# Performance work log

Measured on AMD Instinct MI355X. Metric: run time of the kernel, lower is better.

The kernel has to match this reference:

```python
import jax, jax.numpy as jnp
import numpy as np
from jax import lax

MODES = 16
DEPTH = 8
NPH = 8  # photons = sum(init_state); init_state = [1]*8 + [0]*8
IDX = np.arange(NPH)  # output_indices derived from init_state
PI = np.pi
CHUNK = 4096  # pairs per permanent chunk (memory control, mirrors chunk_subsets idea)


def setup_inputs() -> dict:
    key = jax.random.key(0)
    k1, k2, k3 = jax.random.split(key, 3)
    x = jax.random.normal(k1, (256, 64), dtype=jnp.float32)
    W = jax.random.normal(k2, (120, 64), dtype=jnp.float32) / np.sqrt(64.0)
    b = jax.random.normal(k3, (120,), dtype=jnp.float32) * 0.01
    return {"x": x, "W": W, "b": b}


def _forward(x, W, b):
    N = x.shape[0]
    # fc1 + sigmoid embedding -> angle pairs
    x_emb = jax.nn.sigmoid(x @ W.T + b)              # (N, 120)
    tbu = x_emb.reshape(N, -1, 2)                    # (N, T, 2)
    theta = tbu[:, :, 0] * (PI / 2)
    phi = tbu[:, :, 1] * (2 * PI)
    ct = jnp.cos(theta).astype(jnp.complex64)
    st = jnp.sin(theta).astype(jnp.complex64)
    ep = jnp.exp(1j * phi.astype(jnp.complex64))
    # 2x2 tunable beam-splitter unitaries: [[e^{i phi} c, -s], [e^{i phi} s, c]]
    row0 = jnp.stack([ep * ct, -st], axis=-1)
    row1 = jnp.stack([ep * st, ct], axis=-1)
    blocks = jnp.stack([row0, row1], axis=-2)        # (N, T, 2, 2)

    # Apply block-diagonal layers. Block-diag matmul only mixes row pairs,
    # so update row segments directly instead of building (modes,modes) UBS.
    U = jnp.broadcast_to(jnp.eye(MODES, dtype=jnp.complex64), (N, MODES, MODES))
    nb_even, nb_odd = MODES // 2, (MODES - 2) // 2
    n_before = 0
    for d in range(DEPTH):
        if d % 2 == 0:
            nb, off = nb_even, 0
        else:
            nb, off = nb_odd, 1
        blk = blocks[:, n_before:n_before + nb]                      # (N, nb, 2, 2)
        seg = U[:, off:off + 2 * nb, :].reshape(N, nb, 2, MODES)     # row pairs
        new = jnp.einsum('nkab,nkbm->nkam', blk, seg).reshape(N, 2 * nb, MODES)
        U = U.at[:, off:off + 2 * nb, :].set(new)
        n_before += nb

    # Photonic Gram: K[a,b] = |perm( (U_a^dag U_b)[idx, idx] )|^2.
    # Only the idx-columns of U enter: V = U[:, :, idx], submatrix = V_a^dag V_b.
    V = U[:, :, IDX]                                  # (N, MODES, n)
    G = jnp.einsum('ami,bmj->abij', V.conj(), V)      # (N, N, n, n)

    n = NPH
    subsets = jnp.arange(1, 1 << n)                   # (S,), S = 2^n - 1
    masks = (subsets[:, None] >> jnp.arange(n)[None, :]) & 1   # (S, n)
    signs = (1 - 2 * ((n - masks.sum(axis=1)) & 1)).astype(jnp.complex64)
    maskc = masks.astype(jnp.complex64)

    A = G.reshape(N * N, n, n)
    nc = (N * N) // CHUNK

    def perm_chunk(Ac):  # Ryser: sum_S (-1)^{n-|S|} prod_i sum_{j in S} A_ij
        ss = jnp.einsum('cij,sj->csi', Ac, maskc)     # (c, S, n) subset row-sums
        pr = jnp.prod(ss, axis=2)                     # (c, S)
        return jnp.sum(pr * signs, axis=1)            # (c,)

    perms = lax.map(perm_chunk, A.reshape(nc, CHUNK, n, n)).reshape(N * N)
    K = (jnp.abs(perms) ** 2).astype(jnp.float32).reshape(N, N)
    di = jnp.arange(N)
    K = K.at[di, di].set(1.0)
    return x_emb, K


def reference(x, W, b):
    return _forward(x, W, b)
```

## Files before the change

kernel.cpp:

```cpp
#include <hip/hip_runtime.h>
#include <math.h>

#define NS 256
#define EMB 120
#define NBLK 60
#define MODES 16
#define NPH 8

__device__ __forceinline__ float2 cmul(float2 a, float2 b) {
    float2 r;
    r.x = fmaf(a.x, b.x, -(a.y * b.y));
    r.y = fmaf(a.x, b.y,   a.y * b.x);
    return r;
}

__global__ __launch_bounds__(128) void emb_v_kernel(
    const float* __restrict__ x, const float* __restrict__ W,
    const float* __restrict__ bias, float* __restrict__ out_emb,
    float2* __restrict__ Vws)
{
    const int s = blockIdx.x;
    const int t = threadIdx.x;
    __shared__ float emb[EMB];
    __shared__ float ctA[NBLK], stA[NBLK], exA[NBLK], eyA[NBLK];

    if (t < EMB) {
        const float* xr = x + s * 64;
        const float* wr = W + t * 64;
        float acc = bias[t];
        #pragma unroll
        for (int k = 0; k < 64; ++k) acc = fmaf(xr[k], wr[k], acc);
        float e = 1.0f / (1.0f + expf(-acc));
        emb[t] = e;
        out_emb[s * EMB + t] = e;
    }
    __syncthreads();

    if (t < NBLK) {
        float th = emb[2 * t]     * 1.57079632679489662f;
        float ph = emb[2 * t + 1] * 6.28318530717958648f;
        float st, ct, sp, cp;
        sincosf(th, &st, &ct);
        sincosf(ph, &sp, &cp);
        ctA[t] = ct; stA[t] = st; exA[t] = cp; eyA[t] = sp;
    }
    __syncthreads();

    if (t < NPH) {
        const int c = t;
        float2 u[MODES];
        #pragma unroll
        for (int m = 0; m < MODES; ++m) {
            u[m].x = (m == c) ? 1.0f : 0.0f;
            u[m].y = 0.0f;
        }
        int bi = 0;
        #pragma unroll
        for (int d = 0; d < 8; ++d) {
            const int off = d & 1;
            const int nb = 8 - off;
            #pragma unroll
            for (int k = 0; k < nb; ++k) {
                float ct = ctA[bi], st = stA[bi], ex = exA[bi], ey = eyA[bi];
                ++bi;
                const int r0 = off + 2 * k;
                float2 u0 = u[r0], u1 = u[r0 + 1];
                float2 n0, n1;
                n0.x = ex * ct * u0.x - ey * ct * u0.y - st * u1.x;
                n0.y = ex * ct * u0.y + ey * ct * u0.x - st * u1.y;
                n1.x = ex * st * u0.x - ey * st * u0.y + ct * u1.x;
                n1.y = ex * st * u0.y + ey * st * u0.x + ct * u1.y;
                u[r0] = n0; u[r0 + 1] = n1;
            }
        }
        #pragma unroll
        for (int m = 0; m < MODES; ++m)
            Vws[(s * MODES + m) * NPH + c] = u[m];
    }
}

__global__ __launch_bounds__(256, 1) void perm_kernel(
    const float2* __restrict__ Vws, float* __restrict__ outK)
{
    __shared__ float2 sva[8][132];
    __shared__ float2 svb[8][132];
    __shared__ float2 sG[64][66];

    const int tid = threadIdx.x;
    const int ta = blockIdx.x >> 5;
    const int tb = blockIdx.x & 31;

    const float4* srcA = (const float4*)(Vws + (size_t)ta * 8 * 128);
    const float4* srcB = (const float4*)(Vws + (size_t)tb * 8 * 128);
    #pragma unroll
    for (int r = 0; r < 2; ++r) {
        int idx = r * 256 + tid;
        int row = idx >> 6;
        int c4  = idx & 63;
        *(float4*)&sva[row][c4 * 2] = srcA[idx];
        *(float4*)&svb[row][c4 * 2] = srcB[idx];
    }
    __syncthreads();

    const int p  = tid >> 2;
    const int q  = tid & 3;
    const int pa = p >> 3;
    const int pb = p & 7;

    float2 Ga[2][8];
    #pragma unroll
    for (int i = 0; i < 2; ++i)
        #pragma unroll
        for (int j = 0; j < 8; ++j) { Ga[i][j].x = 0.f; Ga[i][j].y = 0.f; }

    #pragma unroll 1
    for (int m = 0; m < 16; ++m) {
        float4 va4 = *(const float4*)&sva[pa][m * 8 + 2 * q];
        float2 a0; a0.x = va4.x; a0.y = va4.y;
        float2 a1; a1.x = va4.z; a1.y = va4.w;
        float2 vb[8];
        #pragma unroll
        for (int jj = 0; jj < 4; ++jj) {
            float4 b4 = *(const float4*)&svb[pb][m * 8 + 2 * jj];
            vb[2 * jj].x     = b4.x; vb[2 * jj].y     = b4.y;
            vb[2 * jj + 1].x = b4.z; vb[2 * jj + 1].y = b4.w;
        }
        #pragma unroll
        for (int j = 0; j < 8; ++j) {
            Ga[0][j].x = fmaf(a0.x, vb[j].x, fmaf(a0.y, vb[j].y, Ga[0][j].x));
            Ga[0][j].y = fmaf(a0.x, vb[j].y, fmaf(-a0.y, vb[j].x, Ga[0][j].y));
            Ga[1][j].x = fmaf(a1.x, vb[j].x, fmaf(a1.y, vb[j].y, Ga[1][j].x));
            Ga[1][j].y = fmaf(a1.x, vb[j].y, fmaf(-a1.y, vb[j].x, Ga[1][j].y));
        }
    }
    #pragma unroll
    for (int i = 0; i < 2; ++i)
        #pragma unroll
        for (int jj = 0; jj < 4; ++jj) {
            float4 w;
            w.x = Ga[i][2 * jj].x;     w.y = Ga[i][2 * jj].y;
            w.z = Ga[i][2 * jj + 1].x; w.w = Ga[i][2 * jj + 1].y;
            *(float4*)&sG[p][(2 * q + i) * 8 + 2 * jj] = w;
        }
    __syncthreads();

    float2 G[8][8];
    #pragma unroll
    for (int i = 0; i < 8; ++i)
        #pragma unroll
        for (int jj = 0; jj < 4; ++jj) {
            float4 g4 = *(const float4*)&sG[p][i * 8 + 2 * jj];
            G[i][2 * jj].x     = g4.x; G[i][2 * jj].y     = g4.y;
            G[i][2 * jj + 1].x = g4.z; G[i][2 * jj + 1].y = g4.w;
        }

    const float d6 = (q & 1) ? -1.f : 1.f;
    const float d7 = (q & 2) ? -1.f : 1.f;

    float2 rs[8];
    #pragma unroll
    for (int i = 0; i < 8; ++i) {
        float sx = G[i][0].x + G[i][1].x + G[i][2].x + G[i][3].x + G[i][4].x + G[i][5].x;
        float sy = G[i][0].y + G[i][1].y + G[i][2].y + G[i][3].y + G[i][4].y + G[i][5].y;
        sx = fmaf(d6, G[i][6].x, sx); sx = fmaf(d7, G[i][7].x, sx);
        sy = fmaf(d6, G[i][6].y, sy); sy = fmaf(d7, G[i][7].y, sy);
        rs[i].x = sx; rs[i].y = sy;
    }

    float2 acc;

#define PRODTREE(OUT) do {                                            \
        float2 p01 = cmul(rs[0], rs[1]);                              \
        float2 p23 = cmul(rs[2], rs[3]);                              \
        float2 p45 = cmul(rs[4], rs[5]);                              \
        float2 p67 = cmul(rs[6], rs[7]);                              \
        float2 q0  = cmul(p01, p23);                                  \
        float2 q1  = cmul(p45, p67);                                  \
        OUT = cmul(q0, q1);                                           \
    } while (0)

#define UPD(J, S) do {                                                \
        _Pragma("unroll")                                             \
        for (int i = 0; i < 8; ++i) {                                 \
            rs[i].x = fmaf((S), G[i][J].x, rs[i].x);                  \
            rs[i].y = fmaf((S), G[i][J].y, rs[i].y);                  \
        }                                                             \
    } while (0)

#define TERM(TS) do {                                                 \
        float2 pr; PRODTREE(pr);                                      \
        acc.x = fmaf((TS), pr.x, acc.x);                              \
        acc.y = fmaf((TS), pr.y, acc.y);                              \
    } while (0)

    PRODTREE(acc);
    UPD(1, -2.f); TERM(-1.f);
    UPD(2, -2.f); TERM( 1.f);
    UPD(1,  2.f); TERM(-1.f);
    UPD(3, -2.f); TERM( 1.f);
    UPD(1, -2.f); TERM(-1.f);
    UPD(2,  2.f); TERM( 1.f);
    UPD(1,  2.f); TERM(-1.f);
    UPD(4, -2.f); TERM( 1.f);
    UPD(1, -2.f); TERM(-1.f);
    UPD(2, -2.f); TERM( 1.f);
    UPD(1,  2.f); TERM(-1.f);
    UPD(3,  2.f); TERM( 1.f);
    UPD(1, -2.f); TERM(-1.f);
    UPD(2,  2.f); TERM( 1.f);
    UPD(1,  2.f); TERM(-1.f);
    UPD(5, -2.f); TERM( 1.f);
    UPD(1, -2.f); TERM(-1.f);
    UPD(2, -2.f); TERM( 1.f);
    UPD(1,  2.f); TERM(-1.f);
    UPD(3, -2.f); TERM( 1.f);
    UPD(1, -2.f); TERM(-1.f);
    UPD(2,  2.f); TERM( 1.f);
    UPD(1,  2.f); TERM(-1.f);
    UPD(4,  2.f); TERM( 1.f);
    UPD(1, -2.f); TERM(-1.f);
    UPD(2, -2.f); TERM( 1.f);
    UPD(1,  2.f); TERM(-1.f);
    UPD(3,  2.f); TERM( 1.f);
    UPD(1, -2.f); TERM(-1.f);
    UPD(2,  2.f); TERM( 1.f);
    UPD(1,  2.f); TERM(-1.f);
#undef UPD
#undef TERM
#undef PRODTREE

    const float sq = d6 * d7;
    float ax = acc.x * sq, ay = acc.y * sq;
    ax += __shfl_xor(ax, 1); ay += __shfl_xor(ay, 1);
    ax += __shfl_xor(ax, 2); ay += __shfl_xor(ay, 2);

    if (q == 0) {
        const int a = ta * 8 + pa;
        const int b = tb * 8 + pb;
        float K = fmaf(ax, ax, ay * ay) * (1.0f / 16384.0f);
        if (a == b) K = 1.0f;
        outK[a * 256 + b] = K;
    }
}

extern "C" void kernel_launch(void* const* d_in, const int* in_sizes, int n_in,
                              void* d_out, int out_size, void* d_ws, size_t ws_size,
                              hipStream_t stream) {
    const float* x    = (const float*)d_in[0];
    const float* W    = (const float*)d_in[1];
    const float* bias = (const float*)d_in[2];
    float* out     = (float*)d_out;
    float* out_emb = out;
    float* outK    = out + NS * EMB;
    float2* Vws    = (float2*)d_ws;

    emb_v_kernel<<<NS, 128, 0, stream>>>(x, W, bias, out_emb, Vws);
    perm_kernel<<<1024, 256, 0, stream>>>(Vws, outK);
}
```

Measured before the change: 82.34 us.

## Exploit Gram symmetry with triangular tiles and split permanent rows across lanes

Launches only upper-triangular tile pairs (528 blocks) and writes each K value to both (a,b) and (b,a), relying on |perm(G^H)| = |perm(G)| to roughly halve the work. Each pair now uses 8 lanes instead of 4, each holding 4 rows; the 8-row product is completed with a DPP xor-1 exchange, and the final reduction uses DPP plus a shuffle. Shared memory for the V tiles is aliased onto the G buffer. The block is 512 threads with a higher occupancy bound. The cost is an extra cross-lane multiply per Ryser term and some duplicated product work across the lane pair.

Measured after the change: 79.71 us. 3.2% less time.

```diff
diff --git a/kernel.cpp b/kernel.cpp
--- a/kernel.cpp
+++ b/kernel.cpp
@@ -7,11 +7,18 @@
 #define MODES 16
 #define NPH 8
 
-__device__ __forceinline__ float2 cmul(float2 a, float2 b) {
-    float2 r;
-    r.x = fmaf(a.x, b.x, -(a.y * b.y));
-    r.y = fmaf(a.x, b.y,   a.y * b.x);
-    return r;
+#define CMUL(r, a, b) do {                         \
+        (r).x = fmaf((a).x, (b).x, -((a).y * (b).y)); \
+        (r).y = fmaf((a).x, (b).y,  ((a).y * (b).x)); \
+    } while (0)
+
+__device__ __forceinline__ float dpp_xor1(float x) {
+    return __builtin_bit_cast(float,
+        __builtin_amdgcn_mov_dpp(__builtin_bit_cast(int, x), 0xB1, 0xF, 0xF, true));
+}
+__device__ __forceinline__ float dpp_xor2(float x) {
+    return __builtin_bit_cast(float,
+        __builtin_amdgcn_mov_dpp(__builtin_bit_cast(int, x), 0x4E, 0xF, 0xF, true));
 }
 
 __global__ __launch_bounds__(128) void emb_v_kernel(
@@ -79,45 +86,47 @@
     }
 }
 
-__global__ __launch_bounds__(256, 1) void perm_kernel(
+__global__ __launch_bounds__(512, 4) void perm_kernel(
     const float2* __restrict__ Vws, float* __restrict__ outK)
 {
-    __shared__ float2 sva[8][132];
-    __shared__ float2 svb[8][132];
     __shared__ float2 sG[64][66];
+    float2 (*sva)[132] = (float2(*)[132])sG;
+    float2 (*svb)[132] = (float2(*)[132])((char*)sG + 8448);
+
+    const int L = blockIdx.x;
+    int t = (int)((65.0f - sqrtf(4225.0f - 8.0f * (float)L)) * 0.5f);
+    while (t * (65 - t) / 2 > L) --t;
+    while ((t + 1) * (65 - (t + 1)) / 2 <= L) ++t;
+    const int ta = t;
+    const int tb = ta + (L - t * (65 - t) / 2);
 
     const int tid = threadIdx.x;
-    const int ta = blockIdx.x >> 5;
-    const int tb = blockIdx.x & 31;
-
     const float4* srcA = (const float4*)(Vws + (size_t)ta * 8 * 128);
     const float4* srcB = (const float4*)(Vws + (size_t)tb * 8 * 128);
-    #pragma unroll
-    for (int r = 0; r < 2; ++r) {
-        int idx = r * 256 + tid;
-        int row = idx >> 6;
-        int c4  = idx & 63;
-        *(float4*)&sva[row][c4 * 2] = srcA[idx];
-        *(float4*)&svb[row][c4 * 2] = srcB[idx];
-    }
-    __syncthreads();
-
-    const int p  = tid >> 2;
-    const int q  = tid & 3;
+    {
+        const int row = tid >> 6;
+        const int c4  = tid & 63;
+        float4 fa = srcA[tid];
+        float4 fb = srcB[tid];
+        *(float4*)&sva[row][c4 * 2] = fa;
+        *(float4*)&svb[row][c4 * 2] = fb;
+    }
+    __syncthreads();
+
+    const int p  = tid >> 3;
+    const int s  = tid & 7;
+    const int h  = s & 1;
+    const int d  = s >> 1;
     const int pa = p >> 3;
     const int pb = p & 7;
 
-    float2 Ga[2][8];
-    #pragma unroll
-    for (int i = 0; i < 2; ++i)
-        #pragma unroll
-        for (int j = 0; j < 8; ++j) { Ga[i][j].x = 0.f; Ga[i][j].y = 0.f; }
-
-    #pragma unroll 1
+    float2 Gb[8];
+    #pragma unroll
+    for (int j = 0; j < 8; ++j) { Gb[j].x = 0.f; Gb[j].y = 0.f; }
+
+    #pragma unroll 4
     for (int m = 0; m < 16; ++m) {
-        float4 va4 = *(const float4*)&sva[pa][m * 8 + 2 * q];
-        float2 a0; a0.x = va4.x; a0.y = va4.y;
-        float2 a1; a1.x = va4.z; a1.y = va4.w;
+        float2 va = sva[pa][m * 8 + s];
         float2 vb[8];
         #pragma unroll
         for (int jj = 0; jj < 4; ++jj) {
@@ -127,73 +136,74 @@
         }
         #pragma unroll
         for (int j = 0; j < 8; ++j) {
-            Ga[0][j].x = fmaf(a0.x, vb[j].x, fmaf(a0.y, vb[j].y, Ga[0][j].x));
-            Ga[0][j].y = fmaf(a0.x, vb[j].y, fmaf(-a0.y, vb[j].x, Ga[0][j].y));
-            Ga[1][j].x = fmaf(a1.x, vb[j].x, fmaf(a1.y, vb[j].y, Ga[1][j].x));
-            Ga[1][j].y = fmaf(a1.x, vb[j].y, fmaf(-a1.y, vb[j].x, Ga[1][j].y));
-        }
-    }
-    #pragma unroll
-    for (int i = 0; i < 2; ++i)
+            Gb[j].x = fmaf(va.x, vb[j].x, fmaf(va.y, vb[j].y, Gb[j].x));
+            Gb[j].y = fmaf(va.x, vb[j].y, fmaf(-va.y, vb[j].x, Gb[j].y));
+        }
+    }
+    __syncthreads();
+
+    #pragma unroll
+    for (int jj = 0; jj < 4; ++jj) {
+        float4 w;
+        w.x = Gb[2 * jj].x;     w.y = Gb[2 * jj].y;
+        w.z = Gb[2 * jj + 1].x; w.w = Gb[2 * jj + 1].y;
+        *(float4*)&sG[p][s * 8 + 2 * jj] = w;
+    }
+    __syncthreads();
+
+    float2 G[4][8];
+    #pragma unroll
+    for (int k = 0; k < 4; ++k)
         #pragma unroll
         for (int jj = 0; jj < 4; ++jj) {
-            float4 w;
-            w.x = Ga[i][2 * jj].x;     w.y = Ga[i][2 * jj].y;
-            w.z = Ga[i][2 * jj + 1].x; w.w = Ga[i][2 * jj + 1].y;
-            *(float4*)&sG[p][(2 * q + i) * 8 + 2 * jj] = w;
-        }
-    __syncthreads();
-
-    float2 G[8][8];
-    #pragma unroll
-    for (int i = 0; i < 8; ++i)
-        #pragma unroll
-        for (int jj = 0; jj < 4; ++jj) {
-            float4 g4 = *(const float4*)&sG[p][i * 8 + 2 * jj];
-            G[i][2 * jj].x     = g4.x; G[i][2 * jj].y     = g4.y;
-            G[i][2 * jj + 1].x = g4.z; G[i][2 * jj + 1].y = g4.w;
-        }
-
-    const float d6 = (q & 1) ? -1.f : 1.f;
-    const float d7 = (q & 2) ? -1.f : 1.f;
-
-    float2 rs[8];
-    #pragma unroll
-    for (int i = 0; i < 8; ++i) {
-        float sx = G[i][0].x + G[i][1].x + G[i][2].x + G[i][3].x + G[i][4].x + G[i][5].x;
-        float sy = G[i][0].y + G[i][1].y + G[i][2].y + G[i][3].y + G[i][4].y + G[i][5].y;
-        sx = fmaf(d6, G[i][6].x, sx); sx = fmaf(d7, G[i][7].x, sx);
-        sy = fmaf(d6, G[i][6].y, sy); sy = fmaf(d7, G[i][7].y, sy);
+            float4 g4 = *(const float4*)&sG[p][(4 * h + k) * 8 + 2 * jj];
+            G[k][2 * jj].x     = g4.x; G[k][2 * jj].y     = g4.y;
+            G[k][2 * jj + 1].x = g4.z; G[k][2 * jj + 1].y = g4.w;
+        }
+
+    const float s5 = (d & 1) ? -1.f : 1.f;
+    const float s6 = (d & 2) ? -1.f : 1.f;
+    float2 rs[4];
+    #pragma unroll
+    for (int i = 0; i < 4; ++i) {
+        float sx = ((G[i][0].x + G[i][1].x) + (G[i][2].x + G[i][3].x))
+                 + (G[i][4].x + G[i][7].x);
+        float sy = ((G[i][0].y + G[i][1].y) + (G[i][2].y + G[i][3].y))
+                 + (G[i][4].y + G[i][7].y);
+        sx = fmaf(s5, G[i][5].x, sx); sx = fmaf(s6, G[i][6].x, sx);
+        sy = fmaf(s5, G[i][5].y, sy); sy = fmaf(s6, G[i][6].y, sy);
         rs[i].x = sx; rs[i].y = sy;
     }
 
     float2 acc;
 
-#define PRODTREE(OUT) do {                                            \
-        float2 p01 = cmul(rs[0], rs[1]);                              \
-        float2 p23 = cmul(rs[2], rs[3]);                              \
-        float2 p45 = cmul(rs[4], rs[5]);                              \
-        float2 p67 = cmul(rs[6], rs[7]);                              \
-        float2 q0  = cmul(p01, p23);                                  \
-        float2 q1  = cmul(p45, p67);                                  \
-        OUT = cmul(q0, q1);                                           \
-    } while (0)
-
-#define UPD(J, S) do {                                                \
+#define TREE(OUTX, OUTY) do {                                         \
+        float2 m01, m23, hf, fl;                                      \
+        CMUL(m01, rs[0], rs[1]);                                      \
+        CMUL(m23, rs[2], rs[3]);                                      \
+        CMUL(hf, m01, m23);                                           \
+        float2 ot;                                                    \
+        ot.x = dpp_xor1(hf.x);                                        \
+        ot.y = dpp_xor1(hf.y);                                        \
+        CMUL(fl, hf, ot);                                             \
+        OUTX = fl.x; OUTY = fl.y;                                     \
+    } while (0)
+
+#define UPD(J, C) do {                                                \
         _Pragma("unroll")                                             \
-        for (int i = 0; i < 8; ++i) {                                 \
-            rs[i].x = fmaf((S), G[i][J].x, rs[i].x);                  \
-            rs[i].y = fmaf((S), G[i][J].y, rs[i].y);                  \
+        for (int i = 0; i < 4; ++i) {                                 \
+            rs[i].x = fmaf((C), G[i][J].x, rs[i].x);                  \
+            rs[i].y = fmaf((C), G[i][J].y, rs[i].y);                  \
         }                                                             \
     } while (0)
 
 #define TERM(TS) do {                                                 \
-        float2 pr; PRODTREE(pr);                                      \
-        acc.x = fmaf((TS), pr.x, acc.x);                              \
-        acc.y = fmaf((TS), pr.y, acc.y);                              \
-    } while (0)
-
-    PRODTREE(acc);
+        float fx, fy; TREE(fx, fy);                                   \
+        acc.x = fmaf((TS), fx, acc.x);                                \
+        acc.y = fmaf((TS), fy, acc.y);                                \
+    } while (0)
+
+    TREE(acc.x, acc.y);
     UPD(1, -2.f); TERM(-1.f);
     UPD(2, -2.f); TERM( 1.f);
     UPD(1,  2.f); TERM(-1.f);
@@ -209,7 +219,7 @@
     UPD(1, -2.f); TERM(-1.f);
     UPD(2,  2.f); TERM( 1.f);
     UPD(1,  2.f); TERM(-1.f);
-    UPD(5, -2.f); TERM( 1.f);
+    UPD(7, -2.f); TERM( 1.f);
     UPD(1, -2.f); TERM(-1.f);
     UPD(2, -2.f); TERM( 1.f);
     UPD(1,  2.f); TERM(-1.f);
@@ -227,19 +237,22 @@
     UPD(1,  2.f); TERM(-1.f);
 #undef UPD
 #undef TERM
-#undef PRODTREE
-
-    const float sq = d6 * d7;
-    float ax = acc.x * sq, ay = acc.y * sq;
-    ax += __shfl_xor(ax, 1); ay += __shfl_xor(ay, 1);
-    ax += __shfl_xor(ax, 2); ay += __shfl_xor(ay, 2);
-
-    if (q == 0) {
+#undef TREE
+
+    const float sq = s5 * s6;
+    float ax = sq * acc.x, ay = sq * acc.y;
+    ax += dpp_xor2(ax);
+    ay += dpp_xor2(ay);
+    ax += __shfl_xor(ax, 4);
+    ay += __shfl_xor(ay, 4);
+
+    if (s == 0) {
         const int a = ta * 8 + pa;
         const int b = tb * 8 + pb;
         float K = fmaf(ax, ax, ay * ay) * (1.0f / 16384.0f);
         if (a == b) K = 1.0f;
         outK[a * 256 + b] = K;
+        outK[b * 256 + a] = K;
     }
 }
 
@@ -255,5 +268,5 @@
     float2* Vws    = (float2*)d_ws;
 
     emb_v_kernel<<<NS, 128, 0, stream>>>(x, W, bias, out_emb, Vws);
-    perm_kernel<<<1024, 256, 0, stream>>>(Vws, outK);
-}
+    perm_kernel<<<528, 512, 0, stream>>>(Vws, outK);
+}
```
